# Kernel tuning notes

Hardware: AMD Instinct MI355X
Metric: run time of the kernel (lower is better)

Reference implementation:

```python
import jax, jax.numpy as jnp
import numpy as np

N, FEAT, EMB, OUT = 16384, 256, 128, 128


def setup_inputs() -> dict:
    key = jax.random.key(0)
    k1, k2, k3, k4, k5 = jax.random.split(key, 5)
    s1 = 1.0 / np.sqrt(FEAT)
    s2 = 1.0 / np.sqrt(EMB)
    return {
        "x": jax.random.normal(k1, (N, FEAT), dtype=jnp.float32),
        "W1": jax.random.uniform(k2, (FEAT, EMB), jnp.float32, -s1, s1),
        "b1": jax.random.uniform(k3, (EMB,), jnp.float32, -s1, s1),
        "W2": jax.random.uniform(k4, (EMB, OUT), jnp.float32, -s2, s2),
        "b2": jax.random.uniform(k5, (OUT,), jnp.float32, -s2, s2),
    }


def reference(x, W1, b1, W2, b2):
    # projection: [N, feat] -> [N, emb]
    h = x @ W1 + b1
    # dense self-similarity graph: A_ = h h^T  (N x N)
    A_ = h @ h.T
    # degree-style normalization: A_ij -> 2*A_ij / (A_ii + A_jj)
    d = jnp.diagonal(A_)  # [N], == row squared norms of h
    A = 2.0 * A_ / (d[:, None] + d[None, :])
    # degree-normalized aggregation then output MLP + ReLU
    agg = A @ h  # [N, emb]
    return jax.nn.relu(agg @ W2 + b2)
```

## Files before the change

### kernel.cpp

```cpp
#include <hip/hip_runtime.h>
#include <stdint.h>

#define N_TOK 16384
#define FEAT  256
#define EMB   128
#define NQ    13

typedef float  f32x4  __attribute__((ext_vector_type(4)));
typedef __bf16 bf16x8 __attribute__((ext_vector_type(8)));
typedef short  s16x8  __attribute__((ext_vector_type(8)));

__device__ __forceinline__ unsigned short bf16_rne(float f) {
    union { float f; unsigned u; } v; v.f = f;
    unsigned u = v.u;
    return (unsigned short)((u + 0x7FFFu + ((u >> 16) & 1u)) >> 16);
}
__device__ __forceinline__ float bf16_to_f32(unsigned short s) {
    union { unsigned u; float f; } v; v.u = ((unsigned)s) << 16; return v.f;
}
__device__ __forceinline__ void async_cp16(const void* g, void* l) {
    __builtin_amdgcn_global_load_lds(
        (const __attribute__((address_space(1))) unsigned int*)g,
        (__attribute__((address_space(3))) unsigned int*)l, 16, 0, 0);
}

__global__ void k0_transpose(const float* __restrict__ W1, const float* __restrict__ W2,
                             unsigned short* __restrict__ W1T, unsigned short* __restrict__ W2T)
{
    const int tid  = blockIdx.x * blockDim.x + threadIdx.x;
    const int nthr = gridDim.x * blockDim.x;
    for (int i = tid; i < FEAT * EMB; i += nthr) {
        const int r = i >> 7, c = i & 127;
        W1T[c * FEAT + r] = bf16_rne(W1[i]);
    }
    for (int i = tid; i < EMB * EMB; i += nthr) {
        const int r = i >> 7, c = i & 127;
        W2T[c * EMB + r] = bf16_rne(W2[i]);
    }
}

__global__ __launch_bounds__(256) void k1_proj(
    const float* __restrict__ x, const unsigned short* __restrict__ W1T,
    const float* __restrict__ b1,
    unsigned short* __restrict__ h, unsigned short* __restrict__ hT,
    float* __restrict__ dg)
{
    __shared__ __align__(16) unsigned char W1s[65536];
    __shared__ unsigned short ldsT[128 * 68];
    const int lane = threadIdx.x & 63;
    const int wave = threadIdx.x >> 6;
    const int quad = lane >> 4;
    const int l15  = lane & 15;
    const int arow = blockIdx.x * 64 + wave * 16 + l15;

    float4 xv[16];
    #pragma unroll
    for (int ks = 0; ks < 8; ++ks) {
        const float* xp = x + (size_t)arow * FEAT + ks * 32 + quad * 8;
        xv[2 * ks]     = *(const float4*)xp;
        xv[2 * ks + 1] = *(const float4*)(xp + 4);
    }
    #pragma unroll
    for (int c = 0; c < 16; ++c) {
        const int chunk = wave * 16 + c;
        const int row = chunk * 2 + (lane >> 5);
        const int b = (lane & 31) ^ (row & 15);
        async_cp16(W1T + (size_t)row * FEAT + b * 8, W1s + chunk * 1024);
    }
    bf16x8 afr[8];
    #pragma unroll
    for (int ks = 0; ks < 8; ++ks) {
        const float4 xa = xv[2 * ks], xb = xv[2 * ks + 1];
        s16x8 at;
        at[0] = (short)bf16_rne(xa.x); at[1] = (short)bf16_rne(xa.y);
        at[2] = (short)bf16_rne(xa.z); at[3] = (short)bf16_rne(xa.w);
        at[4] = (short)bf16_rne(xb.x); at[5] = (short)bf16_rne(xb.y);
        at[6] = (short)bf16_rne(xb.z); at[7] = (short)bf16_rne(xb.w);
        afr[ks] = __builtin_bit_cast(bf16x8, at);
    }
    __syncthreads();

    const f32x4 zero4 = {0.f, 0.f, 0.f, 0.f};
    f32x4 acc[8];
    #pragma unroll
    for (int n0 = 0; n0 < 8; ++n0) acc[n0] = zero4;
    #pragma unroll
    for (int ks = 0; ks < 8; ++ks)
        #pragma unroll
        for (int n0 = 0; n0 < 8; ++n0) {
            const int n = n0 * 16 + l15;
            const int b = (ks * 4 + quad) ^ (n & 15);
            const bf16x8 bfr = *(const bf16x8*)(W1s + n * 512 + b * 16);
            acc[n0] = __builtin_amdgcn_mfma_f32_16x16x32_bf16(afr[ks], bfr, acc[n0], 0, 0, 0);
        }

    const int rbase = blockIdx.x * 64 + wave * 16 + quad * 4;
    float dpart[4] = {0.f, 0.f, 0.f, 0.f};
    #pragma unroll
    for (int n0 = 0; n0 < 8; ++n0) {
        const int col = n0 * 16 + l15;
        const float bias = b1[col];
        unsigned short hb[4];
        #pragma unroll
        for (int r = 0; r < 4; ++r) {
            const float hv = acc[n0][r] + bias;
            const unsigned short q = bf16_rne(hv);
            hb[r] = q;
            const float bb = bf16_to_f32(q);
            dpart[r] += bb * bb;
            h[(size_t)(rbase + r) * EMB + col] = q;
        }
        ushort4 pk = make_ushort4(hb[0], hb[1], hb[2], hb[3]);
        *(ushort4*)&ldsT[col * 68 + wave * 16 + quad * 4] = pk;
    }
    #pragma unroll
    for (int r = 0; r < 4; ++r) {
        float v = dpart[r];
        v += __shfl_xor(v, 1);
        v += __shfl_xor(v, 2);
        v += __shfl_xor(v, 4);
        v += __shfl_xor(v, 8);
        if (l15 == 0) dg[rbase + r] = v;
    }
    __syncthreads();
    const int rbase0 = blockIdx.x * 64;
    #pragma unroll
    for (int i = 0; i < 4; ++i) {
        const int slot = i * 256 + threadIdx.x;
        const int c    = slot >> 3;
        const int seg  = slot & 7;
        const ushort4 a0 = *(const ushort4*)&ldsT[c * 68 + seg * 8];
        const ushort4 a1 = *(const ushort4*)&ldsT[c * 68 + seg * 8 + 4];
        ushort4 o[2] = {a0, a1};
        *(uint4*)&hT[(size_t)c * N_TOK + rbase0 + seg * 8] = *(const uint4*)o;
    }
}

__global__ __launch_bounds__(256) void k1b_u(const float* __restrict__ dg, float* __restrict__ UT)
{
    const int i = blockIdx.x * 256 + threadIdx.x;
    const float d = dg[i];
    #pragma unroll
    for (int q = 0; q < NQ; ++q) {
        const float tq = (q == 12) ? 0.0f : __expf(0.9f * (float)q - 10.8f);
        UT[(size_t)q * N_TOK + i] = __expf(-tq * d);
    }
}

__global__ __launch_bounds__(256, 2) void k2a_gram(
    const unsigned short* __restrict__ hT, const float* __restrict__ UT,
    float* __restrict__ Gp)
{
    __shared__ __align__(16) unsigned char Rb[32768];
    const int lane = threadIdx.x & 63;
    const int wave = threadIdx.x >> 6;
    const int quad = lane >> 4;
    const int l15  = lane & 15;
    const int q  = blockIdx.x >> 5;
    const int kc = blockIdx.x & 31;
    const int E = wave & 1, F = wave >> 1;

    const f32x4 zero4 = {0.f, 0.f, 0.f, 0.f};
    f32x4 acc[4][4];
    #pragma unroll
    for (int mt = 0; mt < 4; ++mt)
        #pragma unroll
        for (int nt = 0; nt < 4; ++nt) acc[mt][nt] = zero4;

    #pragma unroll 1
    for (int sub = 0; sub < 4; ++sub) {
        const int kwin = kc * 512 + sub * 128;
        __syncthreads();
        #pragma unroll
        for (int c = 0; c < 8; ++c) {
            const int chunk = wave * 8 + c;
            const int row = chunk * 4 + (lane >> 4);
            const int b = (lane & 15) ^ (row & 15);
            async_cp16(hT + (size_t)row * N_TOK + kwin + b * 8, Rb + chunk * 1024);
        }
        __syncthreads();

        #pragma unroll
        for (int ks = 0; ks < 4; ++ks) {
            const int kb = kwin + ks * 32 + quad * 8;
            const float4 ua = *(const float4*)(UT + (size_t)q * N_TOK + kb);
            const float4 ub = *(const float4*)(UT + (size_t)q * N_TOK + kb + 4);
            const float uv[8] = {ua.x, ua.y, ua.z, ua.w, ub.x, ub.y, ub.z, ub.w};
            bf16x8 au[4];
            #pragma unroll
            for (int mt = 0; mt < 4; ++mt) {
                const int re = E * 64 + mt * 16 + l15;
                const int b = (ks * 4 + quad) ^ (re & 15);
                const s16x8 raw = *(const s16x8*)(Rb + re * 256 + b * 16);
                s16x8 sc;
                #pragma unroll
                for (int j = 0; j < 8; ++j)
                    sc[j] = (short)bf16_rne(bf16_to_f32((unsigned short)raw[j]) * uv[j]);
                au[mt] = __builtin_bit_cast(bf16x8, sc);
            }
            #pragma unroll
            for (int nt = 0; nt < 4; ++nt) {
                const int rf = F * 64 + nt * 16 + l15;
                const int b = (ks * 4 + quad) ^ (rf & 15);
                const bf16x8 bfr = *(const bf16x8*)(Rb + rf * 256 + b * 16);
                #pragma unroll
                for (int mt = 0; mt < 4; ++mt)
                    acc[mt][nt] = __builtin_amdgcn_mfma_f32_16x16x32_bf16(au[mt], bfr, acc[mt][nt], 0, 0, 0);
            }
        }
    }

    float* gp = Gp + (size_t)(q * 32 + kc) * (EMB * EMB);
    #pragma unroll
    for (int mt = 0; mt < 4; ++mt)
        #pragma unroll
        for (int nt = 0; nt < 4; ++nt)
            #pragma unroll
            for (int r = 0; r < 4; ++r)
                gp[(size_t)(E * 64 + mt * 16 + quad * 4 + r) * EMB + F * 64 + nt * 16 + l15] = acc[mt][nt][r];
}

__global__ __launch_bounds__(256) void k2r_reduce(const float* __restrict__ Gp, float* __restrict__ G)
{
    const int q   = blockIdx.x >> 6;
    const int idx = (blockIdx.x & 63) * 256 + threadIdx.x;
    float s = 0.f;
    #pragma unroll
    for (int kc = 0; kc < 32; ++kc)
        s += Gp[(size_t)(q * 32 + kc) * (EMB * EMB) + idx];
    G[(size_t)q * (EMB * EMB) + idx] = s;
}

__global__ __launch_bounds__(256) void k2b_gwt(
    const float* __restrict__ G, const unsigned short* __restrict__ W2T,
    unsigned short* __restrict__ GWT)
{
    const int q  = blockIdx.x >> 3;
    const int fs = blockIdx.x & 7;
    const int lane = threadIdx.x & 63;
    const int wave = threadIdx.x >> 6;
    const int quad = lane >> 4;
    const int l15  = lane & 15;
    const float scale = (q == 12) ? 2.0f * __expf(-10.8f)
                                  : 1.8f * __expf(0.9f * (float)q - 10.8f);
    const int fg = fs * 16 + l15;

    const f32x4 zero4 = {0.f, 0.f, 0.f, 0.f};
    f32x4 acc[2];
    acc[0] = zero4; acc[1] = zero4;
    #pragma unroll
    for (int ks = 0; ks < 4; ++ks) {
        const float* p = G + (size_t)q * (EMB * EMB) + (size_t)fg * EMB + ks * 32 + quad * 8;
        const float4 x1 = *(const float4*)p;
        const float4 x2 = *(const float4*)(p + 4);
        const float bv[8] = {x1.x, x1.y, x1.z, x1.w, x2.x, x2.y, x2.z, x2.w};
        s16x8 sb;
        #pragma unroll
        for (int j = 0; j < 8; ++j) sb[j] = (short)bf16_rne(bv[j]);
        const bf16x8 bfr = __builtin_bit_cast(bf16x8, sb);
        #pragma unroll
        for (int mt = 0; mt < 2; ++mt) {
            const int o = wave * 32 + mt * 16 + l15;
            const bf16x8 afr = *(const bf16x8*)(W2T + (size_t)o * EMB + ks * 32 + quad * 8);
            acc[mt] = __builtin_amdgcn_mfma_f32_16x16x32_bf16(afr, bfr, acc[mt], 0, 0, 0);
        }
    }
    #pragma unroll
    for (int mt = 0; mt < 2; ++mt)
        #pragma unroll
        for (int r = 0; r < 4; ++r)
            GWT[(size_t)q * (EMB * EMB) + (size_t)(wave * 32 + mt * 16 + quad * 4 + r) * EMB + fs * 16 + l15]
                = bf16_rne(acc[mt][r] * scale);
}

__global__ __launch_bounds__(256) void k2c_apply(
    const unsigned short* __restrict__ h, const unsigned short* __restrict__ GWT,
    const float* __restrict__ UT, const float* __restrict__ b2,
    float* __restrict__ out)
{
    __shared__ __align__(16) unsigned char Gs[2][32768];
    const int lane = threadIdx.x & 63;
    const int wave = threadIdx.x >> 6;
    const int quad = lane >> 4;
    const int l15  = lane & 15;
    const int i0   = blockIdx.x * 64 + wave * 16;
    const int irow = i0 + l15;

    bf16x8 araw[4];
    #pragma unroll
    for (int ks = 0; ks < 4; ++ks)
        araw[ks] = *(const bf16x8*)(h + (size_t)irow * EMB + ks * 32 + quad * 8);

    const f32x4 zero4 = {0.f, 0.f, 0.f, 0.f};
    f32x4 acc[8];
    #pragma unroll
    for (int nt = 0; nt < 8; ++nt) acc[nt] = zero4;

    #pragma unroll
    for (int c = 0; c < 8; ++c) {
        const int chunk = wave * 8 + c;
        const int row = chunk * 4 + (lane >> 4);
        const int b = (lane & 15) ^ (row & 15);
        async_cp16(GWT + (size_t)row * EMB + b * 8, &Gs[0][chunk * 1024]);
    }
    #pragma unroll 1
    for (int q = 0; q < NQ; ++q) {
        __syncthreads();
        if (q + 1 < NQ) {
            const unsigned short* src = GWT + (size_t)(q + 1) * (EMB * EMB);
            unsigned char* dst = Gs[(q + 1) & 1];
            #pragma unroll
            for (int c = 0; c < 8; ++c) {
                const int chunk = wave * 8 + c;
                const int row = chunk * 4 + (lane >> 4);
                const int b = (lane & 15) ^ (row & 15);
                async_cp16(src + (size_t)row * EMB + b * 8, dst + chunk * 1024);
            }
        }
        const float u = UT[(size_t)q * N_TOK + irow];
        bf16x8 au[4];
        #pragma unroll
        for (int ks = 0; ks < 4; ++ks) {
            const s16x8 raw = __builtin_bit_cast(s16x8, araw[ks]);
            s16x8 sc;
            #pragma unroll
            for (int j = 0; j < 8; ++j)
                sc[j] = (short)bf16_rne(bf16_to_f32((unsigned short)raw[j]) * u);
            au[ks] = __builtin_bit_cast(bf16x8, sc);
        }
        const unsigned char* gb = Gs[q & 1];
        #pragma unroll
        for (int nt = 0; nt < 8; ++nt) {
            const int o = nt * 16 + l15;
            #pragma unroll
            for (int ks = 0; ks < 4; ++ks) {
                const int b = (ks * 4 + quad) ^ (o & 15);
                const bf16x8 bfr = *(const bf16x8*)(gb + o * 256 + b * 16);
                acc[nt] = __builtin_amdgcn_mfma_f32_16x16x32_bf16(au[ks], bfr, acc[nt], 0, 0, 0);
            }
        }
    }

    #pragma unroll
    for (int nt = 0; nt < 8; ++nt) {
        const float bias = b2[nt * 16 + l15];
        #pragma unroll
        for (int r = 0; r < 4; ++r) {
            const float v = acc[nt][r] + bias;
            out[(size_t)(i0 + quad * 4 + r) * EMB + nt * 16 + l15] = v > 0.f ? v : 0.f;
        }
    }
}

extern "C" void kernel_launch(void* const* d_in, const int* in_sizes, int n_in,
                              void* d_out, int out_size, void* d_ws, size_t ws_size,
                              hipStream_t stream) {
    const float* x  = (const float*)d_in[0];
    const float* W1 = (const float*)d_in[1];
    const float* b1 = (const float*)d_in[2];
    const float* W2 = (const float*)d_in[3];
    const float* b2 = (const float*)d_in[4];
    float* out = (float*)d_out;

    char* ws = (char*)d_ws;
    unsigned short* h   = (unsigned short*)(ws);
    unsigned short* hT  = (unsigned short*)(ws + 4194304);
    float*          dg  = (float*)        (ws + 8388608);
    unsigned short* W1T = (unsigned short*)(ws + 8454144);
    unsigned short* W2T = (unsigned short*)(ws + 8519680);
    float*          UT  = (float*)        (ws + 8552448);
    float*          Gp  = (float*)        (ws + 9404416);
    float*          G   = (float*)        (ws + 36667392);
    unsigned short* GWT = (unsigned short*)(ws + 37519360);

    k0_transpose<<<dim3(16),      dim3(256), 0, stream>>>(W1, W2, W1T, W2T);
    k1_proj     <<<dim3(256),     dim3(256), 0, stream>>>(x, W1T, b1, h, hT, dg);
    k1b_u       <<<dim3(64),      dim3(256), 0, stream>>>(dg, UT);
    k2a_gram    <<<dim3(NQ * 32), dim3(256), 0, stream>>>(hT, UT, Gp);
    k2r_reduce  <<<dim3(NQ * 64), dim3(256), 0, stream>>>(Gp, G);
    k2b_gwt     <<<dim3(NQ * 8),  dim3(256), 0, stream>>>(G, W2T, GWT);
    k2c_apply   <<<dim3(256),     dim3(256), 0, stream>>>(h, GWT, UT, b2, out);
}
```

Measured before the change: 135.4 us.

## Fuse U computation into projection, split gram K-range finer, truncate bf16 packing

Removes the separate k1b_u kernel by computing the 13 exponential scale vectors directly in k1_proj from the reduced row norms, one lane per q. Doubles the number of k2a_gram blocks by halving each block's K window, raises its occupancy hint to 3, and makes the partial reduction sum 64 slices. Replaces round-to-nearest bf16 conversion of the scaled operands with truncating pair packing to cut ALU work in the gram and apply kernels. In exchange it grows the partial-sum workspace and reduction traffic and adds truncation error in the scaled operands.

Result: slower. 148.6 us (+9.8%).

```diff
diff --git a/kernel.cpp b/kernel.cpp
--- a/kernel.cpp
+++ b/kernel.cpp
@@ -9,6 +9,7 @@
 typedef float  f32x4  __attribute__((ext_vector_type(4)));
 typedef __bf16 bf16x8 __attribute__((ext_vector_type(8)));
 typedef short  s16x8  __attribute__((ext_vector_type(8)));
+typedef unsigned int u32x4 __attribute__((ext_vector_type(4)));
 
 __device__ __forceinline__ unsigned short bf16_rne(float f) {
     union { float f; unsigned u; } v; v.f = f;
@@ -17,6 +18,10 @@
 }
 __device__ __forceinline__ float bf16_to_f32(unsigned short s) {
     union { unsigned u; float f; } v; v.u = ((unsigned)s) << 16; return v.f;
+}
+__device__ __forceinline__ unsigned pack_trunc(float a, float b) {
+    union { float f; unsigned u; } ua, ub; ua.f = a; ub.f = b;
+    return (ub.u & 0xFFFF0000u) | (ua.u >> 16);
 }
 __device__ __forceinline__ void async_cp16(const void* g, void* l) {
     __builtin_amdgcn_global_load_lds(
@@ -43,7 +48,7 @@
     const float* __restrict__ x, const unsigned short* __restrict__ W1T,
     const float* __restrict__ b1,
     unsigned short* __restrict__ h, unsigned short* __restrict__ hT,
-    float* __restrict__ dg)
+    float* __restrict__ UT)
 {
     __shared__ __align__(16) unsigned char W1s[65536];
     __shared__ unsigned short ldsT[128 * 68];
@@ -113,6 +118,7 @@
         ushort4 pk = make_ushort4(hb[0], hb[1], hb[2], hb[3]);
         *(ushort4*)&ldsT[col * 68 + wave * 16 + quad * 4] = pk;
     }
+    const float tql = __expf(0.9f * (float)l15 - 10.8f);
     #pragma unroll
     for (int r = 0; r < 4; ++r) {
         float v = dpart[r];
@@ -120,7 +126,8 @@
         v += __shfl_xor(v, 2);
         v += __shfl_xor(v, 4);
         v += __shfl_xor(v, 8);
-        if (l15 == 0) dg[rbase + r] = v;
+        if (l15 < 12)       UT[(size_t)l15 * N_TOK + rbase + r] = __expf(-tql * v);
+        else if (l15 == 12) UT[(size_t)12  * N_TOK + rbase + r] = 1.0f;
     }
     __syncthreads();
     const int rbase0 = blockIdx.x * 64;
@@ -136,18 +143,7 @@
     }
 }
 
-__global__ __launch_bounds__(256) void k1b_u(const float* __restrict__ dg, float* __restrict__ UT)
-{
-    const int i = blockIdx.x * 256 + threadIdx.x;
-    const float d = dg[i];
-    #pragma unroll
-    for (int q = 0; q < NQ; ++q) {
-        const float tq = (q == 12) ? 0.0f : __expf(0.9f * (float)q - 10.8f);
-        UT[(size_t)q * N_TOK + i] = __expf(-tq * d);
-    }
-}
-
-__global__ __launch_bounds__(256, 2) void k2a_gram(
+__global__ __launch_bounds__(256, 3) void k2a_gram(
     const unsigned short* __restrict__ hT, const float* __restrict__ UT,
     float* __restrict__ Gp)
 {
@@ -156,8 +152,8 @@
     const int wave = threadIdx.x >> 6;
     const int quad = lane >> 4;
     const int l15  = lane & 15;
-    const int q  = blockIdx.x >> 5;
-    const int kc = blockIdx.x & 31;
+    const int q  = blockIdx.x >> 6;
+    const int kc = blockIdx.x & 63;
     const int E = wave & 1, F = wave >> 1;
 
     const f32x4 zero4 = {0.f, 0.f, 0.f, 0.f};
@@ -168,8 +164,8 @@
         for (int nt = 0; nt < 4; ++nt) acc[mt][nt] = zero4;
 
     #pragma unroll 1
-    for (int sub = 0; sub < 4; ++sub) {
-        const int kwin = kc * 512 + sub * 128;
+    for (int sub = 0; sub < 2; ++sub) {
+        const int kwin = kc * 256 + sub * 128;
         __syncthreads();
         #pragma unroll
         for (int c = 0; c < 8; ++c) {
@@ -192,11 +188,14 @@
                 const int re = E * 64 + mt * 16 + l15;
                 const int b = (ks * 4 + quad) ^ (re & 15);
                 const s16x8 raw = *(const s16x8*)(Rb + re * 256 + b * 16);
-                s16x8 sc;
+                u32x4 ww;
                 #pragma unroll
-                for (int j = 0; j < 8; ++j)
-                    sc[j] = (short)bf16_rne(bf16_to_f32((unsigned short)raw[j]) * uv[j]);
-                au[mt] = __builtin_bit_cast(bf16x8, sc);
+                for (int w = 0; w < 4; ++w) {
+                    const float fa = bf16_to_f32((unsigned short)raw[2 * w])     * uv[2 * w];
+                    const float fb = bf16_to_f32((unsigned short)raw[2 * w + 1]) * uv[2 * w + 1];
+                    ww[w] = pack_trunc(fa, fb);
+                }
+                au[mt] = __builtin_bit_cast(bf16x8, ww);
             }
             #pragma unroll
             for (int nt = 0; nt < 4; ++nt) {
@@ -210,7 +209,7 @@
         }
     }
 
-    float* gp = Gp + (size_t)(q * 32 + kc) * (EMB * EMB);
+    float* gp = Gp + (size_t)(q * 64 + kc) * (EMB * EMB);
     #pragma unroll
     for (int mt = 0; mt < 4; ++mt)
         #pragma unroll
@@ -225,9 +224,9 @@
     const int q   = blockIdx.x >> 6;
     const int idx = (blockIdx.x & 63) * 256 + threadIdx.x;
     float s = 0.f;
-    #pragma unroll
-    for (int kc = 0; kc < 32; ++kc)
-        s += Gp[(size_t)(q * 32 + kc) * (EMB * EMB) + idx];
+    #pragma unroll 8
+    for (int kc = 0; kc < 64; ++kc)
+        s += Gp[(size_t)(q * 64 + kc) * (EMB * EMB) + idx];
     G[(size_t)q * (EMB * EMB) + idx] = s;
 }
 
@@ -322,11 +321,14 @@
         #pragma unroll
         for (int ks = 0; ks < 4; ++ks) {
             const s16x8 raw = __builtin_bit_cast(s16x8, araw[ks]);
-            s16x8 sc;
-            #pragma unroll
-            for (int j = 0; j < 8; ++j)
-                sc[j] = (short)bf16_rne(bf16_to_f32((unsigned short)raw[j]) * u);
-            au[ks] = __builtin_bit_cast(bf16x8, sc);
+            u32x4 ww;
+            #pragma unroll
+            for (int w = 0; w < 4; ++w) {
+                const float fa = bf16_to_f32((unsigned short)raw[2 * w])     * u;
+                const float fb = bf16_to_f32((unsigned short)raw[2 * w + 1]) * u;
+                ww[w] = pack_trunc(fa, fb);
+            }
+            au[ks] = __builtin_bit_cast(bf16x8, ww);
         }
         const unsigned char* gb = Gs[q & 1];
         #pragma unroll
@@ -365,18 +367,16 @@
     char* ws = (char*)d_ws;
     unsigned short* h   = (unsigned short*)(ws);
     unsigned short* hT  = (unsigned short*)(ws + 4194304);
-    float*          dg  = (float*)        (ws + 8388608);
-    unsigned short* W1T = (unsigned short*)(ws + 8454144);
-    unsigned short* W2T = (unsigned short*)(ws + 8519680);
-    float*          UT  = (float*)        (ws + 8552448);
-    float*          Gp  = (float*)        (ws + 9404416);
-    float*          G   = (float*)        (ws + 36667392);
-    unsigned short* GWT = (unsigned short*)(ws + 37519360);
+    unsigned short* W1T = (unsigned short*)(ws + 8388608);
+    unsigned short* W2T = (unsigned short*)(ws + 8454144);
+    float*          UT  = (float*)        (ws + 8486912);
+    float*          Gp  = (float*)        (ws + 9338880);
+    float*          G   = (float*)        (ws + 63864832);
+    unsigned short* GWT = (unsigned short*)(ws + 64716800);
 
     k0_transpose<<<dim3(16),      dim3(256), 0, stream>>>(W1, W2, W1T, W2T);
-    k1_proj     <<<dim3(256),     dim3(256), 0, stream>>>(x, W1T, b1, h, hT, dg);
-    k1b_u       <<<dim3(64),      dim3(256), 0, stream>>>(dg, UT);
-    k2a_gram    <<<dim3(NQ * 32), dim3(256), 0, stream>>>(hT, UT, Gp);
+    k1_proj     <<<dim3(256),     dim3(256), 0, stream>>>(x, W1T, b1, h, hT, UT);
+    k2a_gram    <<<dim3(NQ * 64), dim3(256), 0, stream>>>(hT, UT, Gp);
     k2r_reduce  <<<dim3(NQ * 64), dim3(256), 0, stream>>>(Gp, G);
     k2b_gwt     <<<dim3(NQ * 8),  dim3(256), 0, stream>>>(G, W2T, GWT);
     k2c_apply   <<<dim3(256),     dim3(256), 0, stream>>>(h, GWT, UT, b2, out);
```
